# Kernel optimization log

Measured on AMD Instinct MI355X. Metric: run time of the kernel, lower is better.

## Reference

```python
import jax, jax.numpy as jnp
import numpy as np

B, N, C, H, F = 8, 1024, 128, 4, 32  # batch, nodes, in_channels, heads, n_hidden
EDGE_P = 0.05


def setup_inputs() -> dict:
    key = jax.random.key(0)
    k1, k2, k3, k4 = jax.random.split(key, 4)
    x = jax.random.normal(k1, (B, N, C), dtype=jnp.float32)
    # torch Linear(in=C, out=H*F, bias=False); stored transposed so x @ W works
    W = jax.random.normal(k2, (C, H * F), dtype=jnp.float32) * (1.0 / np.sqrt(C))
    # attn Linear(2F -> 1, bias=False), single weight vector shared across heads
    a = jax.random.normal(k3, (2 * F,), dtype=jnp.float32) * (1.0 / np.sqrt(2 * F))
    # binary adjacency with self-loops so every row has at least one neighbor
    adj = (jax.random.uniform(k4, (N, N)) < EDGE_P).astype(jnp.int32)
    adj = jnp.maximum(adj, jnp.eye(N, dtype=jnp.int32))
    return {"x": x, "W": W, "a": a, "adj": adj}


def reference(x, W, a, adj):
    b, n, _ = x.shape
    f = a.shape[0] // 2
    h = W.shape[1] // f
    g = (x @ W).reshape(b, n, h, f)                      # (B,N,H,F)
    # attn(cat[g_i, g_j]) decomposes exactly: e_ij = lrelu(a1.g_i + a2.g_j)
    s_i = jnp.einsum('bihf,f->bih', g, a[:f])            # source-node term
    s_j = jnp.einsum('bjhf,f->bjh', g, a[f:])            # neighbor term
    e = jax.nn.leaky_relu(s_i[:, :, None, :] + s_j[:, None, :, :],
                          negative_slope=0.2)            # (B,N,N,H)
    e = jnp.where(adj[None, :, :, None] == 0, -jnp.inf, e)
    att = jax.nn.softmax(e, axis=2)                      # softmax over neighbors j
    out = jnp.einsum('bijh,bjhf->bihf', att, g)          # aggregate neighbors
    return out.reshape(b, n, h * f)                      # is_concat=True
```

## Files before the change

kernel.cpp:

```cpp
#include <hip/hip_runtime.h>
#include <hip/hip_bf16.h>
#include <math.h>

#define GB 8
#define GN 1024
#define GC 128
#define GH 4
#define GF 32
#define GHF 128
#define MAXNBR 192
#define XS_STRIDE 136

__global__ __launch_bounds__(256) void gat_gemm(
    const float* __restrict__ x, const float* __restrict__ W,
    const float* __restrict__ a, float* __restrict__ g,
    float* __restrict__ s1, float* __restrict__ s2) {
  __shared__ float xs[32 * XS_STRIDE];
  const int t = threadIdx.x;
  const int base = blockIdx.x * 32;

  const float4* __restrict__ x4 = (const float4*)x;
#pragma unroll
  for (int v = t; v < 1024; v += 256) {
    float4 val = x4[base * 32 + v];
    int r = v >> 5, k4 = v & 31;
    *(float4*)&xs[r * XS_STRIDE + k4 * 4] = val;
  }
  __syncthreads();

  const int cg = t & 31;
  const int rg = t >> 5;
  const int c0 = cg * 4;
  const float4* __restrict__ W4 = (const float4*)W;

  float acc[4][4];
#pragma unroll
  for (int r = 0; r < 4; ++r)
#pragma unroll
    for (int i = 0; i < 4; ++i) acc[r][i] = 0.f;

#pragma unroll 4
  for (int kk = 0; kk < 32; ++kk) {
    const int k = kk * 4;
    float4 wf[4];
#pragma unroll
    for (int dk = 0; dk < 4; ++dk) wf[dk] = W4[(k + dk) * 32 + cg];
#pragma unroll
    for (int r = 0; r < 4; ++r) {
      float4 xf = *(const float4*)&xs[(rg * 4 + r) * XS_STRIDE + k];
#define FMA4(xc, wv)                       \
      acc[r][0] = fmaf(xc, wv.x, acc[r][0]); \
      acc[r][1] = fmaf(xc, wv.y, acc[r][1]); \
      acc[r][2] = fmaf(xc, wv.z, acc[r][2]); \
      acc[r][3] = fmaf(xc, wv.w, acc[r][3]);
      FMA4(xf.x, wf[0]) FMA4(xf.y, wf[1]) FMA4(xf.z, wf[2]) FMA4(xf.w, wf[3])
#undef FMA4
    }
  }

  const int h = cg >> 3;
  const int f0 = (cg & 7) * 4;
  float a1[4], a2[4];
#pragma unroll
  for (int i = 0; i < 4; ++i) { a1[i] = a[f0 + i]; a2[i] = a[GF + f0 + i]; }

#pragma unroll
  for (int r = 0; r < 4; ++r) {
    const int row = base + rg * 4 + r;
    *(float4*)&g[row * GHF + c0] =
        make_float4(acc[r][0], acc[r][1], acc[r][2], acc[r][3]);
    float v1 = acc[r][0] * a1[0] + acc[r][1] * a1[1] + acc[r][2] * a1[2] + acc[r][3] * a1[3];
    float v2 = acc[r][0] * a2[0] + acc[r][1] * a2[1] + acc[r][2] * a2[2] + acc[r][3] * a2[3];
    v1 += __shfl_xor(v1, 1); v1 += __shfl_xor(v1, 2); v1 += __shfl_xor(v1, 4);
    v2 += __shfl_xor(v2, 1); v2 += __shfl_xor(v2, 2); v2 += __shfl_xor(v2, 4);
    if ((cg & 7) == 0) { s1[row * GH + h] = v1; s2[row * GH + h] = v2; }
  }
}

__global__ __launch_bounds__(256) void gat_attn(
    const float* __restrict__ g, const float* __restrict__ s1,
    const float* __restrict__ s2, const int* __restrict__ adj,
    float* __restrict__ out) {
  const int i = blockIdx.x;
  const int t = threadIdx.x;

  __shared__ int nbr[MAXNBR];
  __shared__ float p[GH][MAXNBR];
  __shared__ int cnt;

  if (t == 0) cnt = 0;
  __syncthreads();

  const int* __restrict__ arow = adj + i * GN;
  for (int j = t; j < GN; j += 256) {
    if (arow[j] != 0) {
      int pos = atomicAdd(&cnt, 1);
      if (pos < MAXNBR) nbr[pos] = j;
    }
  }
  __syncthreads();
  const int count = min(cnt, MAXNBR);

  const int h = t >> 6;
  const int lane = t & 63;
  const int kslot = lane >> 3;
  const int f4 = lane & 7;

  for (int b = 0; b < GB; ++b) {
    const float si = s1[(b * GN + i) * GH + h];
    const float* __restrict__ s2b = s2 + (size_t)b * GN * GH;
    const float* __restrict__ gb = g + (size_t)b * GN * GHF;

    float e[3];
    float m = -INFINITY;
#pragma unroll
    for (int ii = 0; ii < 3; ++ii) {
      int k = lane + ii * 64;
      if (k < count) {
        int j = nbr[k];
        float v = si + s2b[j * GH + h];
        v = v > 0.f ? v : 0.2f * v;
        e[ii] = v;
        m = fmaxf(m, v);
      }
    }
#pragma unroll
    for (int mk = 32; mk; mk >>= 1) m = fmaxf(m, __shfl_xor(m, mk));

    float s = 0.f;
#pragma unroll
    for (int ii = 0; ii < 3; ++ii) {
      int k = lane + ii * 64;
      if (k < count) {
        float pv = __expf(e[ii] - m);
        p[h][k] = pv;
        s += pv;
      }
    }
#pragma unroll
    for (int mk = 32; mk; mk >>= 1) s += __shfl_xor(s, mk);

    float4 acc = make_float4(0.f, 0.f, 0.f, 0.f);
    for (int k = kslot; k < count; k += 8) {
      const int j = nbr[k];
      const float pv = p[h][k];
      const float4 gv = *(const float4*)&gb[(j * GH + h) * GF + f4 * 4];
      acc.x = fmaf(pv, gv.x, acc.x);
      acc.y = fmaf(pv, gv.y, acc.y);
      acc.z = fmaf(pv, gv.z, acc.z);
      acc.w = fmaf(pv, gv.w, acc.w);
    }
#pragma unroll
    for (int mk = 8; mk <= 32; mk <<= 1) {
      acc.x += __shfl_xor(acc.x, mk);
      acc.y += __shfl_xor(acc.y, mk);
      acc.z += __shfl_xor(acc.z, mk);
      acc.w += __shfl_xor(acc.w, mk);
    }
    if (kslot == 0) {
      const float inv = 1.f / s;
      *(float4*)&out[((size_t)(b * GN + i) * GH + h) * GF + f4 * 4] =
          make_float4(acc.x * inv, acc.y * inv, acc.z * inv, acc.w * inv);
    }
  }
}

extern "C" void kernel_launch(void* const* d_in, const int* in_sizes, int n_in,
                              void* d_out, int out_size, void* d_ws, size_t ws_size,
                              hipStream_t stream) {
  const float* x = (const float*)d_in[0];
  const float* W = (const float*)d_in[1];
  const float* a = (const float*)d_in[2];
  const int* adj = (const int*)d_in[3];
  float* out = (float*)d_out;

  float* ws = (float*)d_ws;
  float* g = ws;
  float* s1 = g + (size_t)GB * GN * GH * GF;
  float* s2 = s1 + (size_t)GB * GN * GH;

  gat_gemm<<<(GB * GN) / 32, 256, 0, stream>>>(x, W, a, g, s1, s2);
  gat_attn<<<GN, 256, 0, stream>>>(g, s1, s2, adj, out);
}
```

Measured before the change: 118.2 us.

## Build neighbor lists in GEMM kernel and parallelize attention over batch

The adjacency scan moves into the GEMM kernel, which now emits a compacted per-node neighbor list through wave ballot/popcount, so it runs once rather than once per attention block. The attention kernel launches one block per (batch, node) pair instead of looping over the batch inside a block, giving eight times more blocks. The GEMM tile drops to 16 rows per block to double the block count, and the LDS padding stride changes. Costs are extra workspace for the neighbor lists and a serial per-wave ballot loop over 1024 entries in two waves of each GEMM block.

```diff
diff --git a/kernel.cpp b/kernel.cpp
--- a/kernel.cpp
+++ b/kernel.cpp
@@ -9,22 +9,23 @@
 #define GF 32
 #define GHF 128
 #define MAXNBR 192
-#define XS_STRIDE 136
+#define XS_STRIDE 132
 
 __global__ __launch_bounds__(256) void gat_gemm(
     const float* __restrict__ x, const float* __restrict__ W,
-    const float* __restrict__ a, float* __restrict__ g,
-    float* __restrict__ s1, float* __restrict__ s2) {
-  __shared__ float xs[32 * XS_STRIDE];
+    const float* __restrict__ a, const int* __restrict__ adj,
+    float* __restrict__ g, float* __restrict__ s1, float* __restrict__ s2,
+    int* __restrict__ nbrl, int* __restrict__ cntl) {
+  __shared__ float xs[16 * XS_STRIDE];
   const int t = threadIdx.x;
-  const int base = blockIdx.x * 32;
+  const int base = blockIdx.x * 16;
 
   const float4* __restrict__ x4 = (const float4*)x;
-#pragma unroll
-  for (int v = t; v < 1024; v += 256) {
-    float4 val = x4[base * 32 + v];
-    int r = v >> 5, k4 = v & 31;
-    *(float4*)&xs[r * XS_STRIDE + k4 * 4] = val;
+  {
+    float4 v0 = x4[base * 32 + t];
+    float4 v1 = x4[base * 32 + t + 256];
+    *(float4*)&xs[(t >> 5) * XS_STRIDE + (t & 31) * 4] = v0;
+    *(float4*)&xs[((t + 256) >> 5) * XS_STRIDE + (t & 31) * 4] = v1;
   }
   __syncthreads();
 
@@ -33,9 +34,9 @@
   const int c0 = cg * 4;
   const float4* __restrict__ W4 = (const float4*)W;
 
-  float acc[4][4];
+  float acc[2][4];
 #pragma unroll
-  for (int r = 0; r < 4; ++r)
+  for (int r = 0; r < 2; ++r)
 #pragma unroll
     for (int i = 0; i < 4; ++i) acc[r][i] = 0.f;
 
@@ -46,9 +47,9 @@
 #pragma unroll
     for (int dk = 0; dk < 4; ++dk) wf[dk] = W4[(k + dk) * 32 + cg];
 #pragma unroll
-    for (int r = 0; r < 4; ++r) {
-      float4 xf = *(const float4*)&xs[(rg * 4 + r) * XS_STRIDE + k];
-#define FMA4(xc, wv)                       \
+    for (int r = 0; r < 2; ++r) {
+      float4 xf = *(const float4*)&xs[(rg * 2 + r) * XS_STRIDE + k];
+#define FMA4(xc, wv)                         \
       acc[r][0] = fmaf(xc, wv.x, acc[r][0]); \
       acc[r][1] = fmaf(xc, wv.y, acc[r][1]); \
       acc[r][2] = fmaf(xc, wv.z, acc[r][2]); \
@@ -65,8 +66,8 @@
   for (int i = 0; i < 4; ++i) { a1[i] = a[f0 + i]; a2[i] = a[GF + f0 + i]; }
 
 #pragma unroll
-  for (int r = 0; r < 4; ++r) {
-    const int row = base + rg * 4 + r;
+  for (int r = 0; r < 2; ++r) {
+    const int row = base + rg * 2 + r;
     *(float4*)&g[row * GHF + c0] =
         make_float4(acc[r][0], acc[r][1], acc[r][2], acc[r][3]);
     float v1 = acc[r][0] * a1[0] + acc[r][1] * a1[1] + acc[r][2] * a1[2] + acc[r][3] * a1[3];
@@ -75,93 +76,102 @@
     v2 += __shfl_xor(v2, 1); v2 += __shfl_xor(v2, 2); v2 += __shfl_xor(v2, 4);
     if ((cg & 7) == 0) { s1[row * GH + h] = v1; s2[row * GH + h] = v2; }
   }
+
+  const int w = t >> 6;
+  if (w < 2) {
+    const int node = blockIdx.x * 2 + w;
+    const int lane = t & 63;
+    const int* __restrict__ arow = adj + node * GN;
+    int* __restrict__ nrow = nbrl + node * MAXNBR;
+    int pos0 = 0;
+    for (int j0 = 0; j0 < GN; j0 += 64) {
+      int v = arow[j0 + lane];
+      unsigned long long m = __ballot(v != 0);
+      if (v) {
+        int pos = pos0 + __popcll(m & ((1ull << lane) - 1ull));
+        if (pos < MAXNBR) nrow[pos] = j0 + lane;
+      }
+      pos0 += __popcll(m);
+    }
+    if (lane == 0) cntl[node] = min(pos0, MAXNBR);
+  }
 }
 
 __global__ __launch_bounds__(256) void gat_attn(
     const float* __restrict__ g, const float* __restrict__ s1,
-    const float* __restrict__ s2, const int* __restrict__ adj,
-    float* __restrict__ out) {
-  const int i = blockIdx.x;
+    const float* __restrict__ s2, const int* __restrict__ nbrl,
+    const int* __restrict__ cntl, float* __restrict__ out) {
+  const int bi = blockIdx.x;
+  const int b = bi >> 10;
+  const int i = bi & (GN - 1);
   const int t = threadIdx.x;
 
   __shared__ int nbr[MAXNBR];
   __shared__ float p[GH][MAXNBR];
-  __shared__ int cnt;
 
-  if (t == 0) cnt = 0;
+  const int count = cntl[i];
+  if (t < count) nbr[t] = nbrl[i * MAXNBR + t];
   __syncthreads();
-
-  const int* __restrict__ arow = adj + i * GN;
-  for (int j = t; j < GN; j += 256) {
-    if (arow[j] != 0) {
-      int pos = atomicAdd(&cnt, 1);
-      if (pos < MAXNBR) nbr[pos] = j;
-    }
-  }
-  __syncthreads();
-  const int count = min(cnt, MAXNBR);
 
   const int h = t >> 6;
   const int lane = t & 63;
+
+  const float si = s1[(b * GN + i) * GH + h];
+  const float* __restrict__ s2b = s2 + (size_t)b * GN * GH;
+  const float* __restrict__ gb = g + (size_t)b * GN * GHF;
+
+  float e[3];
+  float m = -INFINITY;
+#pragma unroll
+  for (int ii = 0; ii < 3; ++ii) {
+    int k = lane + ii * 64;
+    if (k < count) {
+      int j = nbr[k];
+      float v = si + s2b[j * GH + h];
+      v = v > 0.f ? v : 0.2f * v;
+      e[ii] = v;
+      m = fmaxf(m, v);
+    }
+  }
+#pragma unroll
+  for (int mk = 32; mk; mk >>= 1) m = fmaxf(m, __shfl_xor(m, mk));
+
+  float s = 0.f;
+#pragma unroll
+  for (int ii = 0; ii < 3; ++ii) {
+    int k = lane + ii * 64;
+    if (k < count) {
+      float pv = __expf(e[ii] - m);
+      p[h][k] = pv;
+      s += pv;
+    }
+  }
+#pragma unroll
+  for (int mk = 32; mk; mk >>= 1) s += __shfl_xor(s, mk);
+
   const int kslot = lane >> 3;
   const int f4 = lane & 7;
-
-  for (int b = 0; b < GB; ++b) {
-    const float si = s1[(b * GN + i) * GH + h];
-    const float* __restrict__ s2b = s2 + (size_t)b * GN * GH;
-    const float* __restrict__ gb = g + (size_t)b * GN * GHF;
-
-    float e[3];
-    float m = -INFINITY;
+  float4 acc = make_float4(0.f, 0.f, 0.f, 0.f);
+  for (int k = kslot; k < count; k += 8) {
+    const int j = nbr[k];
+    const float pv = p[h][k];
+    const float4 gv = *(const float4*)&gb[(j * GH + h) * GF + f4 * 4];
+    acc.x = fmaf(pv, gv.x, acc.x);
+    acc.y = fmaf(pv, gv.y, acc.y);
+    acc.z = fmaf(pv, gv.z, acc.z);
+    acc.w = fmaf(pv, gv.w, acc.w);
+  }
 #pragma unroll
-    for (int ii = 0; ii < 3; ++ii) {
-      int k = lane + ii * 64;
-      if (k < count) {
-        int j = nbr[k];
-        float v = si + s2b[j * GH + h];
-        v = v > 0.f ? v : 0.2f * v;
-        e[ii] = v;
-        m = fmaxf(m, v);
-      }
-    }
-#pragma unroll
-    for (int mk = 32; mk; mk >>= 1) m = fmaxf(m, __shfl_xor(m, mk));
-
-    float s = 0.f;
-#pragma unroll
-    for (int ii = 0; ii < 3; ++ii) {
-      int k = lane + ii * 64;
-      if (k < count) {
-        float pv = __expf(e[ii] - m);
-        p[h][k] = pv;
-        s += pv;
-      }
-    }
-#pragma unroll
-    for (int mk = 32; mk; mk >>= 1) s += __shfl_xor(s, mk);
-
-    float4 acc = make_float4(0.f, 0.f, 0.f, 0.f);
-    for (int k = kslot; k < count; k += 8) {
-      const int j = nbr[k];
-      const float pv = p[h][k];
-      const float4 gv = *(const float4*)&gb[(j * GH + h) * GF + f4 * 4];
-      acc.x = fmaf(pv, gv.x, acc.x);
-      acc.y = fmaf(pv, gv.y, acc.y);
-      acc.z = fmaf(pv, gv.z, acc.z);
-      acc.w = fmaf(pv, gv.w, acc.w);
-    }
-#pragma unroll
-    for (int mk = 8; mk <= 32; mk <<= 1) {
-      acc.x += __shfl_xor(acc.x, mk);
-      acc.y += __shfl_xor(acc.y, mk);
-      acc.z += __shfl_xor(acc.z, mk);
-      acc.w += __shfl_xor(acc.w, mk);
-    }
-    if (kslot == 0) {
-      const float inv = 1.f / s;
-      *(float4*)&out[((size_t)(b * GN + i) * GH + h) * GF + f4 * 4] =
-          make_float4(acc.x * inv, acc.y * inv, acc.z * inv, acc.w * inv);
-    }
+  for (int mk = 8; mk <= 32; mk <<= 1) {
+    acc.x += __shfl_xor(acc.x, mk);
+    acc.y += __shfl_xor(acc.y, mk);
+    acc.z += __shfl_xor(acc.z, mk);
+    acc.w += __shfl_xor(acc.w, mk);
+  }
+  if (kslot == 0) {
+    const float inv = 1.f / s;
+    *(float4*)&out[((size_t)(b * GN + i) * GH + h) * GF + f4 * 4] =
+        make_float4(acc.x * inv, acc.y * inv, acc.z * inv, acc.w * inv);
   }
 }
 
@@ -178,7 +188,9 @@
   float* g = ws;
   float* s1 = g + (size_t)GB * GN * GH * GF;
   float* s2 = s1 + (size_t)GB * GN * GH;
+  int* nbrl = (int*)(s2 + (size_t)GB * GN * GH);
+  int* cntl = nbrl + (size_t)GN * MAXNBR;
 
-  gat_gemm<<<(GB * GN) / 32, 256, 0, stream>>>(x, W, a, g, s1, s2);
-  gat_attn<<<GN, 256, 0, stream>>>(g, s1, s2, adj, out);
+  gat_gemm<<<(GB * GN) / 16, 256, 0, stream>>>(x, W, a, adj, g, s1, s2, nbrl, cntl);
+  gat_attn<<<GB * GN, 256, 0, stream>>>(g, s1, s2, nbrl, cntl, out);
 }
```

Result: faster. 99.55 us (-15.8%).
